# Performance work log

Measured on AMD Instinct MI355X. Metric: run time of the kernel, lower is better.

Reference implementation:

```python
import jax, jax.numpy as jnp
import numpy as np
from jax import lax
import math

D_MODEL = 768
EXPAND = 2
D_INNER = EXPAND * D_MODEL          # 1536 (= d_ssm since d_ssm=None)
D_STATE = 128
HEADDIM = 64
NHEADS = D_INNER // HEADDIM         # 24
D_CONV = 4
NGROUPS = 1
CONV_DIM = D_INNER + 2 * NGROUPS * D_STATE            # 1792
D_IN_PROJ = 2 * D_INNER + 2 * NGROUPS * D_STATE + NHEADS  # d_mlp = 0
BATCH, SEQLEN = 2, 2048
EPS = 1e-5


def setup_inputs() -> dict:
    key = jax.random.key(0)
    ks = jax.random.split(key, 8)
    u = jax.random.normal(ks[0], (BATCH, SEQLEN, D_MODEL), dtype=jnp.float32)
    in_proj_w = jax.random.normal(ks[1], (D_IN_PROJ, D_MODEL), dtype=jnp.float32) / math.sqrt(D_MODEL)
    conv_w = jax.random.uniform(ks[2], (CONV_DIM, D_CONV), dtype=jnp.float32, minval=-0.5, maxval=0.5)
    conv_b = jnp.zeros((CONV_DIM,), dtype=jnp.float32)
    # dt_bias = inverse-softplus of dt sampled log-uniform in [1e-3, 1e-1]
    dt = jnp.exp(jax.random.uniform(ks[3], (NHEADS,)) * (math.log(0.1) - math.log(0.001)) + math.log(0.001))
    dt_bias = dt + jnp.log(-jnp.expm1(-dt))
    A_log = jnp.log(jax.random.uniform(ks[4], (NHEADS,), minval=1.0, maxval=16.0))
    D = jnp.ones((NHEADS,), dtype=jnp.float32)
    norm_w = jnp.ones((D_INNER,), dtype=jnp.float32)
    out_proj_w = jax.random.normal(ks[5], (D_MODEL, D_INNER), dtype=jnp.float32) / math.sqrt(D_INNER)
    return {"u": u, "in_proj_w": in_proj_w, "conv_w": conv_w, "conv_b": conv_b,
            "dt_bias": dt_bias, "A_log": A_log, "D": D, "norm_w": norm_w,
            "out_proj_w": out_proj_w}


def _mamba2_forward(u, in_proj_w, conv_w, conv_b, dt_bias, A_log, D, norm_w, out_proj_w):
    b, l, _ = u.shape
    zxbcdt = u @ in_proj_w.T                                   # [b,l,D_IN_PROJ]
    z = zxbcdt[..., :D_INNER]                                  # [b,l,d_ssm]
    xBC = zxbcdt[..., D_INNER:D_INNER + CONV_DIM]              # [b,l,conv_dim]
    dt = zxbcdt[..., D_INNER + CONV_DIM:]                      # [b,l,h]

    # causal depthwise conv1d (pad d_conv-1 left == torch pad both + truncate tail)
    xBC_t = xBC.transpose(0, 2, 1)                             # [b,c,l]
    conv_out = lax.conv_general_dilated(
        xBC_t, conv_w[:, None, :], window_strides=(1,),
        padding=[(D_CONV - 1, 0)], feature_group_count=CONV_DIM,
        dimension_numbers=("NCH", "OIH", "NCH"))
    xBC = jax.nn.silu(conv_out + conv_b[None, :, None]).transpose(0, 2, 1)  # [b,l,c]

    x = xBC[..., :D_INNER].reshape(b, l, NHEADS, HEADDIM)      # [b,l,h,p]
    B = xBC[..., D_INNER:D_INNER + D_STATE]                    # [b,l,n]
    C = xBC[..., D_INNER + D_STATE:]                           # [b,l,n]

    A = -jnp.exp(A_log)                                        # [h]
    dt_dis = jax.nn.softplus(dt + dt_bias)                     # [b,l,h]  (dt_limit=(0,inf) -> no-op clamp)
    dA = jnp.exp(dt_dis * A)                                   # [b,l,h]

    def step(state, inp):
        dA_t, dt_t, B_t, x_t, C_t = inp
        dBx = jnp.einsum("bh,bn,bhp->bhpn", dt_t, B_t, x_t)    # [b,h,p,n]
        state = lax.stop_gradient(state * dA_t[:, :, None, None] + dBx)  # matches torch .detach()
        y_t = jnp.einsum("bhpn,bn->bhp", state, C_t)
        return state, y_t

    xs = (dA.transpose(1, 0, 2), dt_dis.transpose(1, 0, 2),
          B.transpose(1, 0, 2), x.transpose(1, 0, 2, 3), C.transpose(1, 0, 2))
    state0 = jnp.zeros((b, NHEADS, HEADDIM, D_STATE), dtype=u.dtype)
    _, ys = lax.scan(step, state0, xs)                         # [l,b,h,p]
    y = ys.transpose(1, 0, 2, 3) + x * D[None, None, :, None]  # D skip (per-head)
    y = y.reshape(b, l, D_INNER)

    # gated RMSNorm (norm_before_gate=False, group_size = d_ssm)
    yz = y * jax.nn.silu(z)
    y = yz * lax.rsqrt(jnp.mean(yz * yz, axis=-1, keepdims=True) + EPS) * norm_w

    return y @ out_proj_w.T                                    # [b,l,d_model]


def reference(u, in_proj_w, conv_w, conv_b, dt_bias, A_log, D, norm_w, out_proj_w):
    return _mamba2_forward(u, in_proj_w, conv_w, conv_b, dt_bias, A_log, D, norm_w, out_proj_w)
```

## Files before the change

kernel.cpp:

```cpp
#include <hip/hip_runtime.h>
#include <hip/hip_bf16.h>
#include <math.h>

#define D_MODEL   768
#define D_INNER   1536
#define D_STATE   128
#define HEADDIM   64
#define NHEADS    24
#define D_CONV    4
#define CONV_DIM  1792
#define D_IN_PROJ 3352
#define BATCH     2
#define SEQLEN    2048
#define NROWS     (BATCH*SEQLEN)
#define EPS       1e-5f

#define NCHUNK    16
#define CHUNK     128
#define STATE_SZ  (HEADDIM*D_STATE)

#define N1_PAD    3456
#define LDST      136
#define H72       72

typedef __bf16 bf16x8 __attribute__((ext_vector_type(8)));
typedef float  f32x4  __attribute__((ext_vector_type(4)));
typedef short  s16x8  __attribute__((ext_vector_type(8)));

__device__ __forceinline__ short f2b(float f) {
    unsigned u = __float_as_uint(f);
    unsigned r = (u + 0x7FFFu + ((u >> 16) & 1u)) >> 16;
    return (short)r;
}
__device__ __forceinline__ float b2f(short s) {
    return __uint_as_float(((unsigned)(unsigned short)s) << 16);
}

__global__ __launch_bounds__(256) void gemm_bf16_kernel(
    const short* __restrict__ A, const short* __restrict__ W,
    short* __restrict__ C, int K, int Nreal, int NT)
{
    __shared__ short smem[2][2][128][32];
    int flat = blockIdx.x;
    int swz  = (flat & 7) * (gridDim.x >> 3) + (flat >> 3);
    const int m0 = (swz / NT) * 128;
    const int n0 = (swz % NT) * 128;
    const int tid  = threadIdx.x;
    const int lane = tid & 63;
    const int wid  = tid >> 6;
    const int wm = wid >> 1, wn = wid & 1;
    const int lr = lane & 15;
    const int kg = lane >> 4;

    f32x4 acc[4][4];
    #pragma unroll
    for (int i = 0; i < 4; ++i)
        #pragma unroll
        for (int j = 0; j < 4; ++j)
            acc[i][j] = (f32x4){0.f, 0.f, 0.f, 0.f};

    const int srow = (lane >> 2);
    const int scol = (lane & 3) * 8;

    auto STAGE = [&](int buf, int k0) {
        #pragma unroll
        for (int it = 0; it < 2; ++it) {
            int r = wid * 32 + it * 16;
            const short* ga = A + (size_t)(m0 + r + srow) * K + k0 + scol;
            const short* gw = W + (size_t)(n0 + r + srow) * K + k0 + scol;
            __builtin_amdgcn_global_load_lds(
                (const __attribute__((address_space(1))) void*)ga,
                (__attribute__((address_space(3))) void*)&smem[buf][0][r][0], 16, 0, 0);
            __builtin_amdgcn_global_load_lds(
                (const __attribute__((address_space(1))) void*)gw,
                (__attribute__((address_space(3))) void*)&smem[buf][1][r][0], 16, 0, 0);
        }
    };
    auto COMPUTE = [&](int buf) {
        bf16x8 af[4], bf[4];
        #pragma unroll
        for (int i = 0; i < 4; ++i)
            af[i] = *(const bf16x8*)&smem[buf][0][wm * 64 + i * 16 + lr][kg * 8];
        #pragma unroll
        for (int j = 0; j < 4; ++j)
            bf[j] = *(const bf16x8*)&smem[buf][1][wn * 64 + j * 16 + lr][kg * 8];
        #pragma unroll
        for (int i = 0; i < 4; ++i)
            #pragma unroll
            for (int j = 0; j < 4; ++j)
                acc[i][j] = __builtin_amdgcn_mfma_f32_16x16x32_bf16(af[i], bf[j], acc[i][j], 0, 0, 0);
    };

    const int nt = K >> 5;
    STAGE(0, 0);
    __syncthreads();
    int cur = 0;
    for (int t = 0; t < nt - 1; ++t) {
        STAGE(cur ^ 1, (t + 1) << 5);
        COMPUTE(cur);
        __syncthreads();
        cur ^= 1;
    }
    COMPUTE(cur);

    __syncthreads();
    short* eb = &smem[0][0][0][0];
    #pragma unroll
    for (int i = 0; i < 4; ++i)
        #pragma unroll
        for (int j = 0; j < 4; ++j)
            #pragma unroll
            for (int r = 0; r < 4; ++r) {
                int row = wm * 64 + i * 16 + kg * 4 + r;
                int col = wn * 64 + j * 16 + lr;
                eb[row * 128 + col] = f2b(acc[i][j][r]);
            }
    __syncthreads();
    #pragma unroll
    for (int ch = 0; ch < 8; ++ch) {
        int cidx = ch * 256 + tid;
        int row  = cidx >> 4;
        int cp   = cidx & 15;
        int ncol = n0 + cp * 8;
        if (ncol < Nreal)
            *(s16x8*)(C + (size_t)(m0 + row) * Nreal + ncol) =
                *(const s16x8*)(eb + row * 128 + cp * 8);
    }
}

__global__ __launch_bounds__(256) void gemm_bf16_n64_kernel(
    const short* __restrict__ A, const short* __restrict__ W,
    float* __restrict__ C, int K, int N, int NT)
{
    __shared__ short As[2][128][32];
    __shared__ short Ws[2][64][32];
    int flat = blockIdx.x;
    int swz  = (flat & 7) * (gridDim.x >> 3) + (flat >> 3);
    const int m0 = (swz / NT) * 128;
    const int n0 = (swz % NT) * 64;
    const int tid  = threadIdx.x;
    const int lane = tid & 63;
    const int wid  = tid >> 6;
    const int lr = lane & 15;
    const int kg = lane >> 4;

    f32x4 acc[2][4];
    #pragma unroll
    for (int i = 0; i < 2; ++i)
        #pragma unroll
        for (int j = 0; j < 4; ++j)
            acc[i][j] = (f32x4){0.f, 0.f, 0.f, 0.f};

    const int srow = (lane >> 2);
    const int scol = (lane & 3) * 8;

    auto STAGE = [&](int buf, int k0) {
        #pragma unroll
        for (int it = 0; it < 2; ++it) {
            int r = wid * 32 + it * 16;
            const short* ga = A + (size_t)(m0 + r + srow) * K + k0 + scol;
            __builtin_amdgcn_global_load_lds(
                (const __attribute__((address_space(1))) void*)ga,
                (__attribute__((address_space(3))) void*)&As[buf][r][0], 16, 0, 0);
        }
        int r2 = wid * 16;
        const short* gw = W + (size_t)(n0 + r2 + srow) * K + k0 + scol;
        __builtin_amdgcn_global_load_lds(
            (const __attribute__((address_space(1))) void*)gw,
            (__attribute__((address_space(3))) void*)&Ws[buf][r2][0], 16, 0, 0);
    };
    auto COMPUTE = [&](int buf) {
        bf16x8 af[2], bf[4];
        #pragma unroll
        for (int i = 0; i < 2; ++i)
            af[i] = *(const bf16x8*)&As[buf][wid * 32 + i * 16 + lr][kg * 8];
        #pragma unroll
        for (int j = 0; j < 4; ++j)
            bf[j] = *(const bf16x8*)&Ws[buf][j * 16 + lr][kg * 8];
        #pragma unroll
        for (int i = 0; i < 2; ++i)
            #pragma unroll
            for (int j = 0; j < 4; ++j)
                acc[i][j] = __builtin_amdgcn_mfma_f32_16x16x32_bf16(af[i], bf[j], acc[i][j], 0, 0, 0);
    };

    const int nt = K >> 5;
    STAGE(0, 0);
    __syncthreads();
    int cur = 0;
    for (int t = 0; t < nt - 1; ++t) {
        STAGE(cur ^ 1, (t + 1) << 5);
        COMPUTE(cur);
        __syncthreads();
        cur ^= 1;
    }
    COMPUTE(cur);

    #pragma unroll
    for (int i = 0; i < 2; ++i) {
        int mrow = m0 + wid * 32 + i * 16 + kg * 4;
        #pragma unroll
        for (int j = 0; j < 4; ++j) {
            int ncol = n0 + j * 16 + lr;
            #pragma unroll
            for (int r = 0; r < 4; ++r)
                C[(size_t)(mrow + r) * N + ncol] = acc[i][j][r];
        }
    }
}

__global__ __launch_bounds__(256) void cast_bf16_kernel(
    const float* __restrict__ in, short* __restrict__ out, int n4)
{
    int i = blockIdx.x * 256 + threadIdx.x;
    if (i >= n4) return;
    float4 v = *(const float4*)(in + (size_t)i * 4);
    short4 o = make_short4(f2b(v.x), f2b(v.y), f2b(v.z), f2b(v.w));
    *(short4*)(out + (size_t)i * 4) = o;
}

__global__ __launch_bounds__(256) void cast_pad_w1_kernel(
    const float* __restrict__ w, short* __restrict__ wb)
{
    int i = blockIdx.x * 256 + threadIdx.x;
    const int n4 = N1_PAD * D_MODEL / 4;
    if (i >= n4) return;
    size_t base = (size_t)i * 4;
    int row = (int)(base / D_MODEL);
    float4 v = make_float4(0.f, 0.f, 0.f, 0.f);
    if (row < D_IN_PROJ) v = *(const float4*)(w + base);
    short4 o = make_short4(f2b(v.x), f2b(v.y), f2b(v.z), f2b(v.w));
    *(short4*)(wb + base) = o;
}

__global__ __launch_bounds__(256) void conv_silu_kernel(
    const short* __restrict__ zxb, short* __restrict__ cob,
    const float* __restrict__ cw, const float* __restrict__ cb)
{
    const int NG = CONV_DIM / 8;
    int idx = blockIdx.x * 256 + threadIdx.x;
    int g = idx % NG;
    int r = idx / NG;
    int c0 = g * 8;
    int l = r & (SEQLEN - 1);

    float4 w[8];
    #pragma unroll
    for (int e = 0; e < 8; ++e)
        w[e] = *(const float4*)(cw + (size_t)(c0 + e) * 4);

    float acc[8];
    #pragma unroll
    for (int e = 0; e < 8; ++e) acc[e] = cb[c0 + e];

    #pragma unroll
    for (int tap = 0; tap < 4; ++tap) {
        if (l - 3 + tap >= 0) {
            s16x8 v = *(const s16x8*)(zxb + (size_t)(r - 3 + tap) * D_IN_PROJ + D_INNER + c0);
            #pragma unroll
            for (int e = 0; e < 8; ++e) {
                float we = (tap == 0) ? w[e].x : (tap == 1) ? w[e].y : (tap == 2) ? w[e].z : w[e].w;
                acc[e] = fmaf(b2f(v[e]), we, acc[e]);
            }
        }
    }
    s16x8 o;
    #pragma unroll
    for (int e = 0; e < 8; ++e)
        o[e] = f2b(acc[e] / (1.f + expf(-acc[e])));
    *(s16x8*)(cob + (size_t)r * CONV_DIM + c0) = o;
}

__global__ __launch_bounds__(256) void dt_kernel(
    const short* __restrict__ zxb, const float* __restrict__ dt_bias,
    const float* __restrict__ A_log, float* __restrict__ dtb, float* __restrict__ dta)
{
    int idx = blockIdx.x * 256 + threadIdx.x;
    if (idx >= NROWS * NHEADS) return;
    int r = idx / NHEADS, h = idx - r * NHEADS;
    float x = b2f(zxb[(size_t)r * D_IN_PROJ + (D_INNER + CONV_DIM) + h]) + dt_bias[h];
    float sp = (x > 20.f) ? x : log1pf(expf(x));
    float A  = -expf(A_log[h]);
    dtb[idx] = sp;
    dta[idx] = sp * A;
}

__global__ __launch_bounds__(256) void ssd_states(
    const short* __restrict__ co, const float* __restrict__ dtb,
    const float* __restrict__ dta, float* __restrict__ sstate,
    float* __restrict__ cumW, float* __restrict__ clgbuf)
{
    __shared__ short lds[26112];
    __shared__ float clg[128];
    __shared__ float dts[128];

    int t = blockIdx.x;
    int c = t & 15;
    int hb = t >> 4;
    int h = hb % NHEADS;
    int b = hb / NHEADS;
    const int R0 = b * SEQLEN + c * CHUNK;
    const int tid  = threadIdx.x;
    const int lane = tid & 63;
    const int wid  = tid >> 6;
    const int lr = lane & 15;
    const int kg = lane >> 4;
    const short* cobase = co + (size_t)R0 * CONV_DIM;

    if (tid < 128) {
        clg[tid] = dta[(size_t)(R0 + tid) * NHEADS + h];
        dts[tid] = dtb[(size_t)(R0 + tid) * NHEADS + h];
    }
    __syncthreads();
    for (int off = 1; off < 128; off <<= 1) {
        float v = 0.f;
        if (tid < 128 && tid >= off) v = clg[tid - off];
        __syncthreads();
        if (tid < 128) clg[tid] += v;
        __syncthreads();
    }
    const float clgE = clg[127];
    if (tid < 128) {
        size_t o = ((size_t)(b * NHEADS + h)) * SEQLEN + c * CHUNK + tid;
        cumW[o]   = __expf(clg[tid]);
        clgbuf[o] = clg[tid];
    }

    short* Bt = lds;
    short* Xt = lds + 128 * LDST;
    {
        int r = tid >> 1, q = tid & 1;
        float dtv = dts[r];
        const short* xr = cobase + (size_t)r * CONV_DIM + h * HEADDIM + q * 32;
        #pragma unroll
        for (int i = 0; i < 4; ++i) {
            s16x8 xv = *(const s16x8*)(xr + i * 8);
            #pragma unroll
            for (int e = 0; e < 8; ++e)
                Xt[(q * 32 + i * 8 + e) * LDST + r] = f2b(b2f(xv[e]) * dtv);
        }
        float wstr = __expf(clgE - clg[r]);
        const short* br = cobase + (size_t)r * CONV_DIM + D_INNER + q * 64;
        #pragma unroll
        for (int i = 0; i < 8; ++i) {
            s16x8 bv = *(const s16x8*)(br + i * 8);
            #pragma unroll
            for (int e = 0; e < 8; ++e)
                Bt[(q * 64 + i * 8 + e) * LDST + r] = f2b(b2f(bv[e]) * wstr);
        }
    }
    __syncthreads();

    f32x4 acc[4][2];
    #pragma unroll
    for (int i = 0; i < 4; ++i)
        #pragma unroll
        for (int j = 0; j < 2; ++j)
            acc[i][j] = (f32x4){0.f, 0.f, 0.f, 0.f};
    #pragma unroll
    for (int kk = 0; kk < 4; ++kk) {
        bf16x8 af[4], bf[2];
        #pragma unroll
        for (int i = 0; i < 4; ++i)
            af[i] = *(const bf16x8*)(Xt + (i * 16 + lr) * LDST + kk * 32 + kg * 8);
        #pragma unroll
        for (int j = 0; j < 2; ++j)
            bf[j] = *(const bf16x8*)(Bt + (wid * 32 + j * 16 + lr) * LDST + kk * 32 + kg * 8);
        #pragma unroll
        for (int i = 0; i < 4; ++i)
            #pragma unroll
            for (int j = 0; j < 2; ++j)
                acc[i][j] = __builtin_amdgcn_mfma_f32_16x16x32_bf16(af[i], bf[j], acc[i][j], 0, 0, 0);
    }
    float* sbase = sstate + (((size_t)(b * NHEADS + h)) * NCHUNK + c) * STATE_SZ;
    #pragma unroll
    for (int i = 0; i < 4; ++i)
        #pragma unroll
        for (int j = 0; j < 2; ++j)
            #pragma unroll
            for (int r = 0; r < 4; ++r) {
                int p = i * 16 + kg * 4 + r;
                int n = wid * 32 + j * 16 + lr;
                sbase[p * D_STATE + n] = acc[i][j][r];
            }
}

__global__ __launch_bounds__(128) void scan_chunk_prefix(
    const float* __restrict__ cumW, float* __restrict__ sstate)
{
    int blk = blockIdx.x;
    int piece = blk & 15;
    int bh = blk >> 4;
    int tid = threadIdx.x;
    float* base = sstate + (size_t)bh * NCHUNK * STATE_SZ + piece * 512 + tid * 4;
    const float* cw = cumW + (size_t)bh * SEQLEN;
    float4 run = make_float4(0.f, 0.f, 0.f, 0.f);
    for (int c = 0; c < NCHUNK; ++c) {
        float Ac = cw[c * CHUNK + (CHUNK - 1)];
        float* ptr = base + (size_t)c * STATE_SZ;
        float4 loc = *(float4*)ptr;
        *(float4*)ptr = run;
        run.x = fmaf(Ac, run.x, loc.x);
        run.y = fmaf(Ac, run.y, loc.y);
        run.z = fmaf(Ac, run.z, loc.z);
        run.w = fmaf(Ac, run.w, loc.w);
    }
}

__global__ __launch_bounds__(512) void ssd_y(
    const short* __restrict__ co, const float* __restrict__ dtb,
    const float* __restrict__ clgbuf, const float* __restrict__ sstate,
    const float* __restrict__ Dvec, short* __restrict__ ybuf)
{
    __shared__ short lds[26112];
    __shared__ float clg[128];
    __shared__ float dts[128];

    int t = blockIdx.x;
    int c = t & 15;
    int hb = t >> 4;
    int h = hb % NHEADS;
    int b = hb / NHEADS;
    const int R0 = b * SEQLEN + c * CHUNK;
    const int tid  = threadIdx.x;
    const int lane = tid & 63;
    const int wid  = tid >> 6;
    const int lr = lane & 15;
    const int kg = lane >> 4;
    const short* cobase = co + (size_t)R0 * CONV_DIM;

    if (tid < 128) {
        size_t o = ((size_t)(b * NHEADS + h)) * SEQLEN + c * CHUNK + tid;
        clg[tid] = clgbuf[o];
        dts[tid] = dtb[(size_t)(R0 + tid) * NHEADS + h];
    }
    __syncthreads();

    short* CsH = lds;
    short* BsH = lds + 128 * H72;
    const int wmS = wid >> 2, wnS = wid & 3;
    f32x4 accS[4][2];
    #pragma unroll
    for (int i = 0; i < 4; ++i)
        #pragma unroll
        for (int j = 0; j < 2; ++j)
            accS[i][j] = (f32x4){0.f, 0.f, 0.f, 0.f};

    for (int kh = 0; kh < 2; ++kh) {
        {
            int r = tid >> 2, q = tid & 3;
            const short* cr = cobase + (size_t)r * CONV_DIM + (D_INNER + D_STATE) + kh * 64 + q * 16;
            const short* br = cobase + (size_t)r * CONV_DIM + D_INNER + kh * 64 + q * 16;
            *(s16x8*)(CsH + r * H72 + q * 16)     = *(const s16x8*)cr;
            *(s16x8*)(CsH + r * H72 + q * 16 + 8) = *(const s16x8*)(cr + 8);
            *(s16x8*)(BsH + r * H72 + q * 16)     = *(const s16x8*)br;
            *(s16x8*)(BsH + r * H72 + q * 16 + 8) = *(const s16x8*)(br + 8);
        }
        __syncthreads();
        #pragma unroll
        for (int kk = 0; kk < 2; ++kk) {
            bf16x8 af[4], bf[2];
            #pragma unroll
            for (int i = 0; i < 4; ++i)
                af[i] = *(const bf16x8*)(CsH + (wmS * 64 + i * 16 + lr) * H72 + kk * 32 + kg * 8);
            #pragma unroll
            for (int j = 0; j < 2; ++j)
                bf[j] = *(const bf16x8*)(BsH + (wnS * 32 + j * 16 + lr) * H72 + kk * 32 + kg * 8);
            #pragma unroll
            for (int i = 0; i < 4; ++i)
                #pragma unroll
                for (int j = 0; j < 2; ++j)
                    accS[i][j] = __builtin_amdgcn_mfma_f32_16x16x32_bf16(af[i], bf[j], accS[i][j], 0, 0, 0);
        }
        __syncthreads();
    }

    short* Ps = lds;
    short* Xt = lds + 128 * LDST;
    #pragma unroll
    for (int i = 0; i < 4; ++i)
        #pragma unroll
        for (int j = 0; j < 2; ++j)
            #pragma unroll
            for (int r = 0; r < 4; ++r) {
                int l  = wmS * 64 + i * 16 + kg * 4 + r;
                int lp = wnS * 32 + j * 16 + lr;
                float w = (lp <= l) ? __expf(clg[l] - clg[lp]) : 0.f;
                Ps[l * LDST + lp] = f2b(accS[i][j][r] * w);
            }
    if (tid < 256) {
        int r = tid >> 1, q = tid & 1;
        const short* xr = cobase + (size_t)r * CONV_DIM + h * HEADDIM + q * 32;
        float dtv = dts[r];
        #pragma unroll
        for (int i = 0; i < 4; ++i) {
            s16x8 xv = *(const s16x8*)(xr + i * 8);
            #pragma unroll
            for (int e = 0; e < 8; ++e)
                Xt[(q * 32 + i * 8 + e) * LDST + r] = f2b(b2f(xv[e]) * dtv);
        }
    }
    __syncthreads();

    const int wm = wid >> 1, wn = wid & 1;
    f32x4 acc1[2][2];
    #pragma unroll
    for (int i = 0; i < 2; ++i)
        #pragma unroll
        for (int j = 0; j < 2; ++j)
            acc1[i][j] = (f32x4){0.f, 0.f, 0.f, 0.f};
    #pragma unroll
    for (int kk = 0; kk < 4; ++kk) {
        bf16x8 af[2], bf[2];
        #pragma unroll
        for (int i = 0; i < 2; ++i)
            af[i] = *(const bf16x8*)(Ps + (wm * 32 + i * 16 + lr) * LDST + kk * 32 + kg * 8);
        #pragma unroll
        for (int j = 0; j < 2; ++j)
            bf[j] = *(const bf16x8*)(Xt + (wn * 32 + j * 16 + lr) * LDST + kk * 32 + kg * 8);
        #pragma unroll
        for (int i = 0; i < 2; ++i)
            #pragma unroll
            for (int j = 0; j < 2; ++j)
                acc1[i][j] = __builtin_amdgcn_mfma_f32_16x16x32_bf16(af[i], bf[j], acc1[i][j], 0, 0, 0);
    }
    __syncthreads();

    short* Cs = lds;
    short* Sn = lds + 128 * LDST;
    {
        int r = tid >> 2, q = tid & 3;
        const short* cr = cobase + (size_t)r * CONV_DIM + (D_INNER + D_STATE) + q * 32;
        #pragma unroll
        for (int i = 0; i < 4; ++i)
            *(s16x8*)(Cs + r * LDST + q * 32 + i * 8) = *(const s16x8*)(cr + i * 8);
    }
    {
        int r = tid >> 3, q = tid & 7;
        const float* sr = sstate + (((size_t)(b * NHEADS + h)) * NCHUNK + c) * STATE_SZ
                          + (size_t)r * D_STATE + q * 16;
        #pragma unroll
        for (int i = 0; i < 4; ++i) {
            float4 sv = *(const float4*)(sr + i * 4);
            *(short4*)(Sn + r * LDST + q * 16 + i * 4) =
                make_short4(f2b(sv.x), f2b(sv.y), f2b(sv.z), f2b(sv.w));
        }
    }
    __syncthreads();

    f32x4 acc2[2][2];
    #pragma unroll
    for (int i = 0; i < 2; ++i)
        #pragma unroll
        for (int j = 0; j < 2; ++j)
            acc2[i][j] = (f32x4){0.f, 0.f, 0.f, 0.f};
    #pragma unroll
    for (int kk = 0; kk < 4; ++kk) {
        bf16x8 af[2], bf[2];
        #pragma unroll
        for (int i = 0; i < 2; ++i)
            af[i] = *(const bf16x8*)(Cs + (wm * 32 + i * 16 + lr) * LDST + kk * 32 + kg * 8);
        #pragma unroll
        for (int j = 0; j < 2; ++j)
            bf[j] = *(const bf16x8*)(Sn + (wn * 32 + j * 16 + lr) * LDST + kk * 32 + kg * 8);
        #pragma unroll
        for (int i = 0; i < 2; ++i)
            #pragma unroll
            for (int j = 0; j < 2; ++j)
                acc2[i][j] = __builtin_amdgcn_mfma_f32_16x16x32_bf16(af[i], bf[j], acc2[i][j], 0, 0, 0);
    }
    __syncthreads();

    short* yt = lds;
    const float Dh = Dvec[h];
    #pragma unroll
    for (int i = 0; i < 2; ++i)
        #pragma unroll
        for (int j = 0; j < 2; ++j)
            #pragma unroll
            for (int r = 0; r < 4; ++r) {
                int l = wm * 32 + i * 16 + kg * 4 + r;
                int p = wn * 32 + j * 16 + lr;
                float cw = __expf(clg[l]);
                float xval = b2f(cobase[(size_t)l * CONV_DIM + h * HEADDIM + p]);
                yt[l * H72 + p] = f2b(acc1[i][j][r] + cw * acc2[i][j][r] + Dh * xval);
            }
    __syncthreads();
    #pragma unroll
    for (int k = 0; k < 2; ++k) {
        int idx = tid * 2 + k;
        int row = idx >> 3;
        int cp  = idx & 7;
        *(s16x8*)(ybuf + (size_t)(R0 + row) * D_INNER + h * HEADDIM + cp * 8) =
            *(const s16x8*)(yt + row * H72 + cp * 8);
    }
}

__global__ __launch_bounds__(192) void gate_norm_kernel(
    const short* __restrict__ zxb, const short* __restrict__ ybuf,
    const float* __restrict__ norm_w, short* __restrict__ yn)
{
    int r = blockIdx.x;
    int c0 = threadIdx.x * 8;
    s16x8 zv = *(const s16x8*)(zxb + (size_t)r * D_IN_PROJ + c0);
    s16x8 yv = *(const s16x8*)(ybuf + (size_t)r * D_INNER + c0);
    float vals[8];
    float ss = 0.f;
    #pragma unroll
    for (int e = 0; e < 8; ++e) {
        float z = b2f(zv[e]);
        float y = b2f(yv[e]);
        float v = y * (z / (1.f + expf(-z)));
        vals[e] = v;
        ss = fmaf(v, v, ss);
    }
    ss += __shfl_xor(ss, 1);
    ss += __shfl_xor(ss, 2);
    ss += __shfl_xor(ss, 4);
    ss += __shfl_xor(ss, 8);
    ss += __shfl_xor(ss, 16);
    ss += __shfl_xor(ss, 32);
    __shared__ float red[3];
    if ((threadIdx.x & 63) == 0) red[threadIdx.x >> 6] = ss;
    __syncthreads();
    float tot = red[0] + red[1] + red[2];
    float scale = rsqrtf(tot / (float)D_INNER + EPS);
    float4 nw0 = *(const float4*)(norm_w + c0);
    float4 nw1 = *(const float4*)(norm_w + c0 + 4);
    const float nw[8] = {nw0.x, nw0.y, nw0.z, nw0.w, nw1.x, nw1.y, nw1.z, nw1.w};
    s16x8 o;
    #pragma unroll
    for (int e = 0; e < 8; ++e)
        o[e] = f2b(vals[e] * scale * nw[e]);
    *(s16x8*)(yn + (size_t)r * D_INNER + c0) = o;
}

extern "C" void kernel_launch(void* const* d_in, const int* in_sizes, int n_in,
                              void* d_out, int out_size, void* d_ws, size_t ws_size,
                              hipStream_t stream) {
    const float* u          = (const float*)d_in[0];
    const float* in_proj_w  = (const float*)d_in[1];
    const float* conv_w     = (const float*)d_in[2];
    const float* conv_b     = (const float*)d_in[3];
    const float* dt_bias    = (const float*)d_in[4];
    const float* A_log      = (const float*)d_in[5];
    const float* Dvec       = (const float*)d_in[6];
    const float* norm_w     = (const float*)d_in[7];
    const float* out_proj_w = (const float*)d_in[8];
    float* out = (float*)d_out;

    short* zxb    = (short*)d_ws;
    short* cob    = zxb + (size_t)NROWS * D_IN_PROJ;
    float* dtb    = (float*)(cob + (size_t)NROWS * CONV_DIM);
    float* dta    = dtb  + (size_t)NROWS * NHEADS;
    short* ybuf   = (short*)(dta + (size_t)NROWS * NHEADS);
    float* sstate = (float*)(ybuf + (size_t)NROWS * D_INNER);
    float* cumW   = sstate + (size_t)BATCH*NHEADS*NCHUNK*STATE_SZ;
    float* clgbuf = cumW + (size_t)BATCH*NHEADS*SEQLEN;

    short* ub  = (short*)sstate;
    short* w1b = ub + (size_t)NROWS * D_MODEL;
    short* ynb = (short*)sstate;
    short* w2b = zxb;

    cast_bf16_kernel<<<(NROWS*D_MODEL/4 + 255)/256, 256, 0, stream>>>(u, ub, NROWS*D_MODEL/4);
    cast_pad_w1_kernel<<<(N1_PAD*D_MODEL/4 + 255)/256, 256, 0, stream>>>(in_proj_w, w1b);
    gemm_bf16_kernel<<<(NROWS/128)*(N1_PAD/128), 256, 0, stream>>>(ub, w1b, zxb, D_MODEL, D_IN_PROJ, N1_PAD/128);
    conv_silu_kernel<<<NROWS*(CONV_DIM/8)/256, 256, 0, stream>>>(zxb, cob, conv_w, conv_b);
    dt_kernel<<<(NROWS*NHEADS + 255)/256, 256, 0, stream>>>(zxb, dt_bias, A_log, dtb, dta);
    ssd_states<<<BATCH*NHEADS*NCHUNK, 256, 0, stream>>>(cob, dtb, dta, sstate, cumW, clgbuf);
    scan_chunk_prefix<<<BATCH*NHEADS*16, 128, 0, stream>>>(cumW, sstate);
    ssd_y<<<BATCH*NHEADS*NCHUNK, 512, 0, stream>>>(cob, dtb, clgbuf, sstate, Dvec, ybuf);
    gate_norm_kernel<<<NROWS, 192, 0, stream>>>(zxb, ybuf, norm_w, ynb);
    cast_bf16_kernel<<<(D_MODEL*D_INNER/4 + 255)/256, 256, 0, stream>>>(out_proj_w, w2b, D_MODEL*D_INNER/4);
    gemm_bf16_n64_kernel<<<(NROWS/128)*(D_MODEL/64), 256, 0, stream>>>(ynb, w2b, out, D_INNER, D_MODEL, D_MODEL/64);
}
```

Baseline: 236.0 us.

## Fuse cast and conv/dt kernels; merge C·state GEMM into ssd_y CB loop

The three fp32-to-bf16 casts (u, in_proj_w, out_proj_w) become one launch, and out_proj_w's bf16 copy moves to its own workspace region so it can be written early. The conv+SiLU and dt/softplus kernels are merged into a single launch that splits the work by block index. In ssd_y, the C·initial-state MFMA is computed in the same k-loop that already stages C for the C·B^T product, with the state staged into LDS there. This removes a separate C reload, a staging phase and two barriers. The main costs removed are launch overhead and redundant LDS staging; the trade-offs are more register pressure in ssd_y and a larger workspace footprint that must fit the allocated buffer.

```diff
diff --git a/kernel.cpp b/kernel.cpp
--- a/kernel.cpp
+++ b/kernel.cpp
@@ -209,80 +209,87 @@
     }
 }
 
-__global__ __launch_bounds__(256) void cast_bf16_kernel(
-    const float* __restrict__ in, short* __restrict__ out, int n4)
+#define N4_U   (NROWS*D_MODEL/4)
+#define N4_W1  (N1_PAD*D_MODEL/4)
+#define N4_W2  (D_MODEL*D_INNER/4)
+__global__ __launch_bounds__(256) void fused_cast_kernel(
+    const float* __restrict__ u, const float* __restrict__ w1,
+    const float* __restrict__ w2,
+    short* __restrict__ ub, short* __restrict__ w1b, short* __restrict__ w2b)
 {
     int i = blockIdx.x * 256 + threadIdx.x;
-    if (i >= n4) return;
-    float4 v = *(const float4*)(in + (size_t)i * 4);
-    short4 o = make_short4(f2b(v.x), f2b(v.y), f2b(v.z), f2b(v.w));
-    *(short4*)(out + (size_t)i * 4) = o;
-}
-
-__global__ __launch_bounds__(256) void cast_pad_w1_kernel(
-    const float* __restrict__ w, short* __restrict__ wb)
-{
-    int i = blockIdx.x * 256 + threadIdx.x;
-    const int n4 = N1_PAD * D_MODEL / 4;
-    if (i >= n4) return;
-    size_t base = (size_t)i * 4;
-    int row = (int)(base / D_MODEL);
-    float4 v = make_float4(0.f, 0.f, 0.f, 0.f);
-    if (row < D_IN_PROJ) v = *(const float4*)(w + base);
-    short4 o = make_short4(f2b(v.x), f2b(v.y), f2b(v.z), f2b(v.w));
-    *(short4*)(wb + base) = o;
-}
-
-__global__ __launch_bounds__(256) void conv_silu_kernel(
+    const float* src;
+    short* dst;
+    size_t off;
+    if (i < N4_U) {
+        src = u; dst = ub; off = (size_t)i * 4;
+        float4 v = *(const float4*)(src + off);
+        *(short4*)(dst + off) = make_short4(f2b(v.x), f2b(v.y), f2b(v.z), f2b(v.w));
+    } else if (i < N4_U + N4_W1) {
+        int j = i - N4_U;
+        off = (size_t)j * 4;
+        int row = (int)(off / D_MODEL);
+        float4 v = make_float4(0.f, 0.f, 0.f, 0.f);
+        if (row < D_IN_PROJ) v = *(const float4*)(w1 + off);
+        *(short4*)(w1b + off) = make_short4(f2b(v.x), f2b(v.y), f2b(v.z), f2b(v.w));
+    } else if (i < N4_U + N4_W1 + N4_W2) {
+        int j = i - N4_U - N4_W1;
+        off = (size_t)j * 4;
+        float4 v = *(const float4*)(w2 + off);
+        *(short4*)(w2b + off) = make_short4(f2b(v.x), f2b(v.y), f2b(v.z), f2b(v.w));
+    }
+}
+
+#define NG      (CONV_DIM/8)
+#define CONVB   (NROWS*NG/256)
+#define DTB     (NROWS*NHEADS/256)
+__global__ __launch_bounds__(256) void conv_dt_kernel(
     const short* __restrict__ zxb, short* __restrict__ cob,
-    const float* __restrict__ cw, const float* __restrict__ cb)
-{
-    const int NG = CONV_DIM / 8;
-    int idx = blockIdx.x * 256 + threadIdx.x;
-    int g = idx % NG;
-    int r = idx / NG;
-    int c0 = g * 8;
-    int l = r & (SEQLEN - 1);
-
-    float4 w[8];
-    #pragma unroll
-    for (int e = 0; e < 8; ++e)
-        w[e] = *(const float4*)(cw + (size_t)(c0 + e) * 4);
-
-    float acc[8];
-    #pragma unroll
-    for (int e = 0; e < 8; ++e) acc[e] = cb[c0 + e];
-
-    #pragma unroll
-    for (int tap = 0; tap < 4; ++tap) {
-        if (l - 3 + tap >= 0) {
-            s16x8 v = *(const s16x8*)(zxb + (size_t)(r - 3 + tap) * D_IN_PROJ + D_INNER + c0);
-            #pragma unroll
-            for (int e = 0; e < 8; ++e) {
-                float we = (tap == 0) ? w[e].x : (tap == 1) ? w[e].y : (tap == 2) ? w[e].z : w[e].w;
-                acc[e] = fmaf(b2f(v[e]), we, acc[e]);
+    const float* __restrict__ cw, const float* __restrict__ cb,
+    const float* __restrict__ dt_bias, const float* __restrict__ A_log,
+    float* __restrict__ dtb, float* __restrict__ dta)
+{
+    if (blockIdx.x < CONVB) {
+        int idx = blockIdx.x * 256 + threadIdx.x;
+        int g = idx % NG;
+        int r = idx / NG;
+        int c0 = g * 8;
+        int l = r & (SEQLEN - 1);
+
+        float4 w[8];
+        #pragma unroll
+        for (int e = 0; e < 8; ++e)
+            w[e] = *(const float4*)(cw + (size_t)(c0 + e) * 4);
+
+        float acc[8];
+        #pragma unroll
+        for (int e = 0; e < 8; ++e) acc[e] = cb[c0 + e];
+
+        #pragma unroll
+        for (int tap = 0; tap < 4; ++tap) {
+            if (l - 3 + tap >= 0) {
+                s16x8 v = *(const s16x8*)(zxb + (size_t)(r - 3 + tap) * D_IN_PROJ + D_INNER + c0);
+                #pragma unroll
+                for (int e = 0; e < 8; ++e) {
+                    float we = (tap == 0) ? w[e].x : (tap == 1) ? w[e].y : (tap == 2) ? w[e].z : w[e].w;
+                    acc[e] = fmaf(b2f(v[e]), we, acc[e]);
+                }
             }
         }
-    }
-    s16x8 o;
-    #pragma unroll
-    for (int e = 0; e < 8; ++e)
-        o[e] = f2b(acc[e] / (1.f + expf(-acc[e])));
-    *(s16x8*)(cob + (size_t)r * CONV_DIM + c0) = o;
-}
-
-__global__ __launch_bounds__(256) void dt_kernel(
-    const short* __restrict__ zxb, const float* __restrict__ dt_bias,
-    const float* __restrict__ A_log, float* __restrict__ dtb, float* __restrict__ dta)
-{
-    int idx = blockIdx.x * 256 + threadIdx.x;
-    if (idx >= NROWS * NHEADS) return;
-    int r = idx / NHEADS, h = idx - r * NHEADS;
-    float x = b2f(zxb[(size_t)r * D_IN_PROJ + (D_INNER + CONV_DIM) + h]) + dt_bias[h];
-    float sp = (x > 20.f) ? x : log1pf(expf(x));
-    float A  = -expf(A_log[h]);
-    dtb[idx] = sp;
-    dta[idx] = sp * A;
+        s16x8 o;
+        #pragma unroll
+        for (int e = 0; e < 8; ++e)
+            o[e] = f2b(acc[e] / (1.f + expf(-acc[e])));
+        *(s16x8*)(cob + (size_t)r * CONV_DIM + c0) = o;
+    } else {
+        int idx = (blockIdx.x - CONVB) * 256 + threadIdx.x;
+        int r = idx / NHEADS, h = idx - r * NHEADS;
+        float x = b2f(zxb[(size_t)r * D_IN_PROJ + (D_INNER + CONV_DIM) + h]) + dt_bias[h];
+        float sp = (x > 20.f) ? x : log1pf(expf(x));
+        float A  = -expf(A_log[h]);
+        dtb[idx] = sp;
+        dta[idx] = sp * A;
+    }
 }
 
 __global__ __launch_bounds__(256) void ssd_states(
@@ -438,13 +445,23 @@
 
     short* CsH = lds;
     short* BsH = lds + 128 * H72;
+    short* SnH = lds + 256 * H72;
     const int wmS = wid >> 2, wnS = wid & 3;
+    const int wm  = wid >> 1, wn  = wid & 1;
+    const float* sinit = sstate + (((size_t)(b * NHEADS + h)) * NCHUNK + c) * STATE_SZ;
+
     f32x4 accS[4][2];
+    f32x4 accY2[2][2];
     #pragma unroll
     for (int i = 0; i < 4; ++i)
         #pragma unroll
         for (int j = 0; j < 2; ++j)
             accS[i][j] = (f32x4){0.f, 0.f, 0.f, 0.f};
+    #pragma unroll
+    for (int i = 0; i < 2; ++i)
+        #pragma unroll
+        for (int j = 0; j < 2; ++j)
+            accY2[i][j] = (f32x4){0.f, 0.f, 0.f, 0.f};
 
     for (int kh = 0; kh < 2; ++kh) {
         {
@@ -455,6 +472,14 @@
             *(s16x8*)(CsH + r * H72 + q * 16 + 8) = *(const s16x8*)(cr + 8);
             *(s16x8*)(BsH + r * H72 + q * 16)     = *(const s16x8*)br;
             *(s16x8*)(BsH + r * H72 + q * 16 + 8) = *(const s16x8*)(br + 8);
+            int rp = tid >> 3, qp = tid & 7;
+            const float* sr = sinit + (size_t)rp * D_STATE + kh * 64 + qp * 8;
+            float4 s0 = *(const float4*)sr;
+            float4 s1 = *(const float4*)(sr + 4);
+            s16x8 sv;
+            sv[0] = f2b(s0.x); sv[1] = f2b(s0.y); sv[2] = f2b(s0.z); sv[3] = f2b(s0.w);
+            sv[4] = f2b(s1.x); sv[5] = f2b(s1.y); sv[6] = f2b(s1.z); sv[7] = f2b(s1.w);
+            *(s16x8*)(SnH + rp * H72 + qp * 8) = sv;
         }
         __syncthreads();
         #pragma unroll
@@ -471,6 +496,18 @@
                 #pragma unroll
                 for (int j = 0; j < 2; ++j)
                     accS[i][j] = __builtin_amdgcn_mfma_f32_16x16x32_bf16(af[i], bf[j], accS[i][j], 0, 0, 0);
+            bf16x8 af2[2], bf2[2];
+            #pragma unroll
+            for (int i = 0; i < 2; ++i)
+                af2[i] = *(const bf16x8*)(CsH + (wm * 32 + i * 16 + lr) * H72 + kk * 32 + kg * 8);
+            #pragma unroll
+            for (int j = 0; j < 2; ++j)
+                bf2[j] = *(const bf16x8*)(SnH + (wn * 32 + j * 16 + lr) * H72 + kk * 32 + kg * 8);
+            #pragma unroll
+            for (int i = 0; i < 2; ++i)
+                #pragma unroll
+                for (int j = 0; j < 2; ++j)
+                    accY2[i][j] = __builtin_amdgcn_mfma_f32_16x16x32_bf16(af2[i], bf2[j], accY2[i][j], 0, 0, 0);
         }
         __syncthreads();
     }
@@ -502,7 +539,6 @@
     }
     __syncthreads();
 
-    const int wm = wid >> 1, wn = wid & 1;
     f32x4 acc1[2][2];
     #pragma unroll
     for (int i = 0; i < 2; ++i)
@@ -523,51 +559,6 @@
             #pragma unroll
             for (int j = 0; j < 2; ++j)
                 acc1[i][j] = __builtin_amdgcn_mfma_f32_16x16x32_bf16(af[i], bf[j], acc1[i][j], 0, 0, 0);
-    }
-    __syncthreads();
-
-    short* Cs = lds;
-    short* Sn = lds + 128 * LDST;
-    {
-        int r = tid >> 2, q = tid & 3;
-        const short* cr = cobase + (size_t)r * CONV_DIM + (D_INNER + D_STATE) + q * 32;
-        #pragma unroll
-        for (int i = 0; i < 4; ++i)
-            *(s16x8*)(Cs + r * LDST + q * 32 + i * 8) = *(const s16x8*)(cr + i * 8);
-    }
-    {
-        int r = tid >> 3, q = tid & 7;
-        const float* sr = sstate + (((size_t)(b * NHEADS + h)) * NCHUNK + c) * STATE_SZ
-                          + (size_t)r * D_STATE + q * 16;
-        #pragma unroll
-        for (int i = 0; i < 4; ++i) {
-            float4 sv = *(const float4*)(sr + i * 4);
-            *(short4*)(Sn + r * LDST + q * 16 + i * 4) =
-                make_short4(f2b(sv.x), f2b(sv.y), f2b(sv.z), f2b(sv.w));
-        }
-    }
-    __syncthreads();
-
-    f32x4 acc2[2][2];
-    #pragma unroll
-    for (int i = 0; i < 2; ++i)
-        #pragma unroll
-        for (int j = 0; j < 2; ++j)
-            acc2[i][j] = (f32x4){0.f, 0.f, 0.f, 0.f};
-    #pragma unroll
-    for (int kk = 0; kk < 4; ++kk) {
-        bf16x8 af[2], bf[2];
-        #pragma unroll
-        for (int i = 0; i < 2; ++i)
-            af[i] = *(const bf16x8*)(Cs + (wm * 32 + i * 16 + lr) * LDST + kk * 32 + kg * 8);
-        #pragma unroll
-        for (int j = 0; j < 2; ++j)
-            bf[j] = *(const bf16x8*)(Sn + (wn * 32 + j * 16 + lr) * LDST + kk * 32 + kg * 8);
-        #pragma unroll
-        for (int i = 0; i < 2; ++i)
-            #pragma unroll
-            for (int j = 0; j < 2; ++j)
-                acc2[i][j] = __builtin_amdgcn_mfma_f32_16x16x32_bf16(af[i], bf[j], acc2[i][j], 0, 0, 0);
     }
     __syncthreads();
 
@@ -583,7 +574,7 @@
                 int p = wn * 32 + j * 16 + lr;
                 float cw = __expf(clg[l]);
                 float xval = b2f(cobase[(size_t)l * CONV_DIM + h * HEADDIM + p]);
-                yt[l * H72 + p] = f2b(acc1[i][j][r] + cw * acc2[i][j][r] + Dh * xval);
+                yt[l * H72 + p] = f2b(acc1[i][j][r] + cw * accY2[i][j][r] + Dh * xval);
             }
     __syncthreads();
     #pragma unroll
@@ -657,21 +648,21 @@
     float* sstate = (float*)(ybuf + (size_t)NROWS * D_INNER);
     float* cumW   = sstate + (size_t)BATCH*NHEADS*NCHUNK*STATE_SZ;
     float* clgbuf = cumW + (size_t)BATCH*NHEADS*SEQLEN;
+    short* w2b    = (short*)(clgbuf + (size_t)BATCH*NHEADS*SEQLEN);
 
     short* ub  = (short*)sstate;
     short* w1b = ub + (size_t)NROWS * D_MODEL;
     short* ynb = (short*)sstate;
-    short* w2b = zxb;
-
-    cast_bf16_kernel<<<(NROWS*D_MODEL/4 + 255)/256, 256, 0, stream>>>(u, ub, NROWS*D_MODEL/4);
-    cast_pad_w1_kernel<<<(N1_PAD*D_MODEL/4 + 255)/256, 256, 0, stream>>>(in_proj_w, w1b);
+
+    {
+        int total = N4_U + N4_W1 + N4_W2;
+        fused_cast_kernel<<<(total + 255)/256, 256, 0, stream>>>(u, in_proj_w, out_proj_w, ub, w1b, w2b);
+    }
     gemm_bf16_kernel<<<(NROWS/128)*(N1_PAD/128), 256, 0, stream>>>(ub, w1b, zxb, D_MODEL, D_IN_PROJ, N1_PAD/128);
-    conv_silu_kernel<<<NROWS*(CONV_DIM/8)/256, 256, 0, stream>>>(zxb, cob, conv_w, conv_b);
-    dt_kernel<<<(NROWS*NHEADS + 255)/256, 256, 0, stream>>>(zxb, dt_bias, A_log, dtb, dta);
+    conv_dt_kernel<<<CONVB + DTB, 256, 0, stream>>>(zxb, cob, conv_w, conv_b, dt_bias, A_log, dtb, dta);
     ssd_states<<<BATCH*NHEADS*NCHUNK, 256, 0, stream>>>(cob, dtb, dta, sstate, cumW, clgbuf);
     scan_chunk_prefix<<<BATCH*NHEADS*16, 128, 0, stream>>>(cumW, sstate);
     ssd_y<<<BATCH*NHEADS*NCHUNK, 512, 0, stream>>>(cob, dtb, clgbuf, sstate, Dvec, ybuf);
     gate_norm_kernel<<<NROWS, 192, 0, stream>>>(zxb, ybuf, norm_w, ynb);
-    cast_bf16_kernel<<<(D_MODEL*D_INNER/4 + 255)/256, 256, 0, stream>>>(out_proj_w, w2b, D_MODEL*D_INNER/4);
     gemm_bf16_n64_kernel<<<(NROWS/128)*(D_MODEL/64), 256, 0, stream>>>(ynb, w2b, out, D_INNER, D_MODEL, D_MODEL/64);
 }
```

Result: no change. 239.1 us (+1.3%).
